# Kernel optimization log

Hardware: AMD Instinct MI355X
Metric: run time of the kernel (lower is better)

## Reference

```python
import jax, jax.numpy as jnp
import numpy as np

B, T, K, H = 2, 2048, 1024, 16


def setup_inputs() -> dict:
    key = jax.random.key(0)
    ks = jax.random.split(key, 9)
    sc = 0.02
    return {
        "x": jax.random.normal(ks[0], (B, T, K), dtype=jnp.float32),
        "Wq_w": jax.random.normal(ks[1], (K, K), dtype=jnp.float32) * sc,
        "Wq_b": jax.random.normal(ks[2], (K,), dtype=jnp.float32) * sc,
        "Wk_w": jax.random.normal(ks[3], (K, K), dtype=jnp.float32) * sc,
        "Wk_b": jax.random.normal(ks[4], (K,), dtype=jnp.float32) * sc,
        "Wv_w": jax.random.normal(ks[5], (K, K), dtype=jnp.float32) * sc,
        "Wv_b": jax.random.normal(ks[6], (K,), dtype=jnp.float32) * sc,
        "Wo_w": jax.random.normal(ks[7], (K, K), dtype=jnp.float32) * sc,
        "Wo_b": jax.random.normal(ks[8], (K,), dtype=jnp.float32) * sc,
    }


def reference(x, Wq_w, Wq_b, Wk_w, Wk_b, Wv_w, Wv_b, Wo_w, Wo_b):
    b, t, k = x.shape
    h = H
    s = k // h
    # nn.Linear: y = x @ W^T + b
    q = x @ Wq_w.T + Wq_b
    kk = x @ Wk_w.T + Wk_b
    v = x @ Wv_w.T + Wv_b
    # [b, t, h, s] -> [b, h, t, s]
    q = q.reshape(b, t, h, s).transpose(0, 2, 1, 3)
    kk = kk.reshape(b, t, h, s).transpose(0, 2, 1, 3)
    v = v.reshape(b, t, h, s).transpose(0, 2, 1, 3)
    # scores [b, h, t, t]
    dot = jnp.einsum("bhqd,bhkd->bhqk", q, kk)
    # causal mask: upper triangle (offset=1) set to -inf BEFORE scaling
    causal = jnp.tril(jnp.ones((t, t), dtype=bool))
    dot = jnp.where(causal, dot, -jnp.inf)
    # NOTE: original scales by sqrt(k) (full model dim), not sqrt(head_dim)
    dot = dot / jnp.sqrt(jnp.asarray(k, dot.dtype))
    attn = jax.nn.softmax(dot, axis=-1)
    out = jnp.einsum("bhqk,bhkd->bhqd", attn, v)  # [b, h, t, s]
    out = out.transpose(0, 2, 1, 3).reshape(b, t, k)
    return out @ Wo_w.T + Wo_b
```

## Files before the change

### kernel.cpp

```cpp
#include <hip/hip_runtime.h>

typedef unsigned short u16;
typedef unsigned int u32;
typedef __bf16 bf16x8 __attribute__((ext_vector_type(8)));
typedef float f32x4 __attribute__((ext_vector_type(4)));
typedef unsigned short u16x8 __attribute__((ext_vector_type(8)));

#define B_ 2
#define T_ 2048
#define K_ 1024
#define H_ 16
#define S_ 64
#define MKC 4194304
#define QSCALE 0.04508422f

__device__ __forceinline__ u16 f2bf(float f) {
  unsigned int u = __builtin_bit_cast(unsigned int, f);
  u += 0x7fffu + ((u >> 16) & 1u);
  return (u16)(u >> 16);
}

__device__ __forceinline__ f32x4 MFMA(bf16x8 a, bf16x8 b, f32x4 c) {
  return __builtin_amdgcn_mfma_f32_16x16x32_bf16(a, b, c, 0, 0, 0);
}

__device__ __forceinline__ void gld16(const void* g, void* l) {
  __builtin_amdgcn_global_load_lds((const __attribute__((address_space(1))) void*)g,
                                   (__attribute__((address_space(3))) void*)l, 16, 0, 0);
}

__global__ __launch_bounds__(256) void cvt_all(const float* __restrict__ x,
                                               const float* __restrict__ W0,
                                               const float* __restrict__ W1,
                                               const float* __restrict__ W2,
                                               const float* __restrict__ W3,
                                               u16* __restrict__ xb,
                                               u16* __restrict__ wb) {
  const int i = blockIdx.x * 256 + threadIdx.x;
  const float* src;
  u16* dst;
  if (i < 524288) {
    src = x + (size_t)i * 8;
    dst = xb + (size_t)i * 8;
  } else {
    const int j = i - 524288;
    const int sel = j >> 17;
    const float* W = sel == 0 ? W0 : sel == 1 ? W1 : sel == 2 ? W2 : W3;
    src = W + (size_t)(j & 131071) * 8;
    dst = wb + (size_t)j * 8;
  }
  const float4* s = (const float4*)src;
  float4 f0 = s[0], f1 = s[1];
  u16x8 p;
  p[0] = f2bf(f0.x); p[1] = f2bf(f0.y); p[2] = f2bf(f0.z); p[3] = f2bf(f0.w);
  p[4] = f2bf(f1.x); p[5] = f2bf(f1.y); p[6] = f2bf(f1.z); p[7] = f2bf(f1.w);
  *(u16x8*)dst = p;
}

template <int OMODE, int BN>
__global__ __launch_bounds__(256) void gemm16(const u16* __restrict__ A,
                                              const u16* __restrict__ Bm,
                                              const float* __restrict__ b0,
                                              const float* __restrict__ b1,
                                              const float* __restrict__ b2,
                                              void* __restrict__ C0,
                                              int M, int N, int K) {
  constexpr int NF = BN / 32;
  __shared__ u16 As[128 * 32];
  __shared__ u16 Bs[BN * 32];
  const int bm = blockIdx.x * 128;
  const int bn = blockIdx.y * BN;
  const int tid = threadIdx.x;
  const int w = tid >> 6, lane = tid & 63;
  const int wr = (w >> 1) * 64, wc = (w & 1) * (BN / 2);
  const int lr = lane & 15, g = lane >> 4;
  const int lk = g * 8;
  const int srow = lane >> 2, scol = (lane & 3) * 8;

  f32x4 acc[4][NF] = {};

  for (int k0 = 0; k0 < K; k0 += 32) {
#pragma unroll
    for (int i = 0; i < 2; ++i) {
      const int rbase = (i * 4 + w) * 16;
      gld16(A + (size_t)(bm + rbase + srow) * K + k0 + scol, &As[rbase * 32]);
    }
#pragma unroll
    for (int i = 0; i < BN / 64; ++i) {
      const int rbase = (i * 4 + w) * 16;
      gld16(Bm + (size_t)(bn + rbase + srow) * K + k0 + scol, &Bs[rbase * 32]);
    }
    asm volatile("s_waitcnt vmcnt(0)" ::: "memory");
    __syncthreads();
    bf16x8 af[4], bfr[NF];
#pragma unroll
    for (int m = 0; m < 4; ++m)
      af[m] = *(const bf16x8*)&As[(wr + m * 16 + lr) * 32 + lk];
#pragma unroll
    for (int n = 0; n < NF; ++n)
      bfr[n] = *(const bf16x8*)&Bs[(wc + n * 16 + lr) * 32 + lk];
    __builtin_amdgcn_s_setprio(1);
#pragma unroll
    for (int m = 0; m < 4; ++m)
#pragma unroll
      for (int n = 0; n < NF; ++n)
        acc[m][n] = MFMA(af[m], bfr[n], acc[m][n]);
    __builtin_amdgcn_s_setprio(0);
    __syncthreads();
  }

  const int sel = (OMODE == 2) ? 0 : (bn >> 10);
  const float* bp = (OMODE == 2) ? b0 : (sel == 0 ? b0 : sel == 1 ? b1 : b2);
#pragma unroll
  for (int n = 0; n < NF; ++n) {
    const int col = bn + wc + n * 16 + lr;
    const float bv = bp[(OMODE == 2) ? col : (col & 1023)];
#pragma unroll
    for (int m = 0; m < 4; ++m) {
#pragma unroll
      for (int r = 0; r < 4; ++r) {
        const int row = bm + wr + m * 16 + g * 4 + r;
        float v = acc[m][n][r] + bv;
        if (OMODE == 2) {
          ((float*)C0)[(size_t)row * N + col] = v;
        } else {
          u16* dst = (u16*)C0;
          const int cc = col & 1023;
          if (sel == 2) {
            const int bb = row >> 11, t = row & 2047, hh = cc >> 6, ss = cc & 63;
            dst[(size_t)2 * MKC + (((size_t)(bb * H_ + hh) * S_ + ss) << 11) + t] = f2bf(v);
          } else {
            if (sel == 0) v *= QSCALE;
            dst[(size_t)sel * MKC + (size_t)row * 1024 + cc] = f2bf(v);
          }
        }
      }
    }
  }
}

__global__ __launch_bounds__(256) void attn_fwd(const u16* __restrict__ Q,
                                                const u16* __restrict__ Kb,
                                                const u16* __restrict__ Vt,
                                                u16* __restrict__ O) {
  __shared__ u16 Ks[2][64 * 64];
  __shared__ u16 Vs[2][64 * 64];
  __shared__ u32 Ps[4][16 * 32];
  const int tid = threadIdx.x;
  const int w = tid >> 6, lane = tid & 63;
  const int qh = lane & 15;
  const int g = lane >> 4;
  const int bh = blockIdx.x;
  const int b = bh >> 4, h = bh & 15;
  const int yy = blockIdx.y, t7 = yy & 7, kq = yy >> 3;
  const int qtile = (kq == 0) ? t7 : (kq == 1) ? (15 - t7) : (kq == 2) ? (16 + t7) : (31 - t7);
  const int qb = qtile * 64;
  const int qw = qb + w * 16;
  const int myq = qw + qh;

  const size_t qoff = (size_t)(b * T_ + qw + qh) * K_ + h * S_ + g * 8;
  const bf16x8 bq0 = *(const bf16x8*)(Q + qoff);
  const bf16x8 bq1 = *(const bf16x8*)(Q + qoff + 32);

  const int srow = lane >> 3;
  const int sslot = (lane & 7) ^ srow;
  auto stage = [&](int buf, int k0) {
#pragma unroll
    for (int i = 0; i < 2; ++i) {
      const int rbase = w * 16 + i * 8;
      gld16(Kb + (size_t)(b * T_ + k0 + rbase + srow) * K_ + h * S_ + sslot * 8,
            &Ks[buf][rbase * 64]);
      gld16(Vt + (size_t)(bh * S_ + rbase + srow) * T_ + k0 + sslot * 8,
            &Vs[buf][rbase * 64]);
    }
  };

  const int nk = qtile + 1;
  stage(0, 0);
  asm volatile("s_waitcnt vmcnt(0)" ::: "memory");
  __syncthreads();

  float m = -INFINITY, lsum = 0.f;
  f32x4 o[4] = {};
  u32* pr = &Ps[w][qh * 32];
  const int sx = (qh & 7) << 2;
  const int ksw = qh & 7;

  for (int kt = 0; kt < nk; ++kt) {
    const int k0 = kt * 64;
    const int cur = kt & 1;
    if (kt + 1 < nk) stage(cur ^ 1, k0 + 64);

    f32x4 s[4] = {};
    __builtin_amdgcn_s_setprio(1);
#pragma unroll
    for (int a = 0; a < 4; ++a) {
      const u16* kr = &Ks[cur][(a * 16 + qh) * 64];
      const bf16x8 kf0 = *(const bf16x8*)(kr + ((g ^ ksw) * 8));
      const bf16x8 kf1 = *(const bf16x8*)(kr + (((4 + g) ^ ksw) * 8));
      s[a] = MFMA(kf0, bq0, s[a]);
      s[a] = MFMA(kf1, bq1, s[a]);
    }
    __builtin_amdgcn_s_setprio(0);

    float p[4][4];
    float vmax = -INFINITY;
    if (k0 + 63 > qw) {
#pragma unroll
      for (int a = 0; a < 4; ++a)
#pragma unroll
        for (int r = 0; r < 4; ++r) {
          const int kv = k0 + a * 16 + g * 4 + r;
          const float v = (kv <= myq) ? s[a][r] : -INFINITY;
          p[a][r] = v;
          vmax = fmaxf(vmax, v);
        }
    } else {
#pragma unroll
      for (int a = 0; a < 4; ++a)
#pragma unroll
        for (int r = 0; r < 4; ++r) {
          p[a][r] = s[a][r];
          vmax = fmaxf(vmax, s[a][r]);
        }
    }
    vmax = fmaxf(vmax, __shfl_xor(vmax, 16));
    vmax = fmaxf(vmax, __shfl_xor(vmax, 32));

    if (__any(vmax > m + 11.5f)) {
      const float mnew = fmaxf(m, vmax);
      const float alpha = __builtin_amdgcn_exp2f(m - mnew);
      m = mnew;
      lsum *= alpha;
      float aR[4];
#pragma unroll
      for (int r = 0; r < 4; ++r) aR[r] = __shfl(alpha, 4 * g + r);
#pragma unroll
      for (int n = 0; n < 4; ++n)
#pragma unroll
        for (int r = 0; r < 4; ++r) o[n][r] *= aR[r];
    }

    float ls = 0.f;
#pragma unroll
    for (int a = 0; a < 4; ++a)
#pragma unroll
      for (int r = 0; r < 4; ++r) {
        p[a][r] = __builtin_amdgcn_exp2f(p[a][r] - m);
        ls += p[a][r];
      }
    ls += __shfl_xor(ls, 16);
    ls += __shfl_xor(ls, 32);
    lsum += ls;

#pragma unroll
    for (int a = 0; a < 4; ++a) {
      u32 u0, u1;
      asm("v_cvt_pk_bf16_f32 %0, %1, %2" : "=v"(u0) : "v"(p[a][0]), "v"(p[a][1]));
      asm("v_cvt_pk_bf16_f32 %0, %1, %2" : "=v"(u1) : "v"(p[a][2]), "v"(p[a][3]));
      uint2 uu; uu.x = u0; uu.y = u1;
      *(uint2*)&pr[(8 * a + 2 * g) ^ sx] = uu;
    }
    __builtin_amdgcn_s_setprio(1);
#pragma unroll
    for (int c = 0; c < 2; ++c) {
      const bf16x8 pa = *(const bf16x8*)&pr[(16 * c + 4 * g) ^ sx];
#pragma unroll
      for (int n = 0; n < 4; ++n) {
        const bf16x8 vf =
            *(const bf16x8*)(&Vs[cur][(16 * n + qh) * 64] + (((c * 4 + g) ^ ksw) * 8));
        o[n] = MFMA(pa, vf, o[n]);
      }
    }
    __builtin_amdgcn_s_setprio(0);

    asm volatile("s_waitcnt vmcnt(0)" ::: "memory");
    __syncthreads();
  }

  const float inv = 1.f / lsum;
  float iR[4];
#pragma unroll
  for (int r = 0; r < 4; ++r) iR[r] = __shfl(inv, 4 * g + r);
#pragma unroll
  for (int r = 0; r < 4; ++r) {
    const size_t row = (size_t)(b * T_ + qw + 4 * g + r);
#pragma unroll
    for (int n = 0; n < 4; ++n)
      O[row * K_ + h * S_ + n * 16 + qh] = f2bf(o[n][r] * iR[r]);
  }
}

extern "C" void kernel_launch(void* const* d_in, const int* in_sizes, int n_in,
                              void* d_out, int out_size, void* d_ws, size_t ws_size,
                              hipStream_t stream) {
  (void)in_sizes; (void)n_in; (void)out_size; (void)ws_size;
  const float* x  = (const float*)d_in[0];
  const float* Wq = (const float*)d_in[1];
  const float* bq = (const float*)d_in[2];
  const float* Wk = (const float*)d_in[3];
  const float* bk = (const float*)d_in[4];
  const float* Wv = (const float*)d_in[5];
  const float* bv = (const float*)d_in[6];
  const float* Wo = (const float*)d_in[7];
  const float* bo = (const float*)d_in[8];
  float* out = (float*)d_out;

  const size_t MK = (size_t)MKC;
  const size_t WK = (size_t)K_ * K_;
  u16* Qb  = (u16*)d_ws;
  u16* Kbf = Qb + MK;
  u16* Vtb = Kbf + MK;
  u16* AO  = Vtb + MK;
  u16* xb  = AO + MK;
  u16* Wqkv = xb + MK;
  u16* Wob  = Wqkv + 3 * WK;

  dim3 blk(256);
  cvt_all<<<dim3(4096), blk, 0, stream>>>(x, Wq, Wk, Wv, Wo, xb, Wqkv);
  gemm16<3, 128><<<dim3(32, 24), blk, 0, stream>>>(xb, Wqkv, bq, bk, bv, Qb,
                                                   B_ * T_, 3 * K_, K_);
  attn_fwd<<<dim3(B_ * H_, T_ / 64), blk, 0, stream>>>(Qb, Kbf, Vtb, AO);
  gemm16<2, 64><<<dim3(32, 16), blk, 0, stream>>>(AO, Wob, bo, bo, bo, out,
                                                  B_ * T_, K_, K_);
}
```

Before: 116.3 us.

## Double-buffer GEMM shared tiles and widen attention KV tile to 128

After: 116.4 us. About the same (+0.0%).

```diff
diff --git a/kernel.cpp b/kernel.cpp
--- a/kernel.cpp
+++ b/kernel.cpp
@@ -66,8 +66,8 @@
                                               void* __restrict__ C0,
                                               int M, int N, int K) {
   constexpr int NF = BN / 32;
-  __shared__ u16 As[128 * 32];
-  __shared__ u16 Bs[BN * 32];
+  __shared__ u16 As[2][128 * 32];
+  __shared__ u16 Bs[2][BN * 32];
   const int bm = blockIdx.x * 128;
   const int bn = blockIdx.y * BN;
   const int tid = threadIdx.x;
@@ -79,33 +79,39 @@
 
   f32x4 acc[4][NF] = {};
 
-  for (int k0 = 0; k0 < K; k0 += 32) {
+  auto stg = [&](int buf, int k0) {
 #pragma unroll
     for (int i = 0; i < 2; ++i) {
       const int rbase = (i * 4 + w) * 16;
-      gld16(A + (size_t)(bm + rbase + srow) * K + k0 + scol, &As[rbase * 32]);
+      gld16(A + (size_t)(bm + rbase + srow) * K + k0 + scol, &As[buf][rbase * 32]);
     }
 #pragma unroll
     for (int i = 0; i < BN / 64; ++i) {
       const int rbase = (i * 4 + w) * 16;
-      gld16(Bm + (size_t)(bn + rbase + srow) * K + k0 + scol, &Bs[rbase * 32]);
-    }
-    asm volatile("s_waitcnt vmcnt(0)" ::: "memory");
-    __syncthreads();
+      gld16(Bm + (size_t)(bn + rbase + srow) * K + k0 + scol, &Bs[buf][rbase * 32]);
+    }
+  };
+
+  stg(0, 0);
+  asm volatile("s_waitcnt vmcnt(0)" ::: "memory");
+  __syncthreads();
+
+  for (int k0 = 0; k0 < K; k0 += 32) {
+    const int buf = (k0 >> 5) & 1;
+    if (k0 + 32 < K) stg(buf ^ 1, k0 + 32);
     bf16x8 af[4], bfr[NF];
 #pragma unroll
     for (int m = 0; m < 4; ++m)
-      af[m] = *(const bf16x8*)&As[(wr + m * 16 + lr) * 32 + lk];
+      af[m] = *(const bf16x8*)&As[buf][(wr + m * 16 + lr) * 32 + lk];
 #pragma unroll
     for (int n = 0; n < NF; ++n)
-      bfr[n] = *(const bf16x8*)&Bs[(wc + n * 16 + lr) * 32 + lk];
-    __builtin_amdgcn_s_setprio(1);
+      bfr[n] = *(const bf16x8*)&Bs[buf][(wc + n * 16 + lr) * 32 + lk];
 #pragma unroll
     for (int m = 0; m < 4; ++m)
 #pragma unroll
       for (int n = 0; n < NF; ++n)
         acc[m][n] = MFMA(af[m], bfr[n], acc[m][n]);
-    __builtin_amdgcn_s_setprio(0);
+    asm volatile("s_waitcnt vmcnt(0)" ::: "memory");
     __syncthreads();
   }
 
@@ -143,9 +149,9 @@
                                                 const u16* __restrict__ Kb,
                                                 const u16* __restrict__ Vt,
                                                 u16* __restrict__ O) {
-  __shared__ u16 Ks[2][64 * 64];
-  __shared__ u16 Vs[2][64 * 64];
-  __shared__ u32 Ps[4][16 * 32];
+  __shared__ u16 Ks[2][128 * 64];
+  __shared__ u16 Vs[2][64 * 128];
+  __shared__ u32 Ps[4][16 * 64];
   const int tid = threadIdx.x;
   const int w = tid >> 6, lane = tid & 63;
   const int qh = lane & 15;
@@ -153,7 +159,7 @@
   const int bh = blockIdx.x;
   const int b = bh >> 4, h = bh & 15;
   const int yy = blockIdx.y, t7 = yy & 7, kq = yy >> 3;
-  const int qtile = (kq == 0) ? t7 : (kq == 1) ? (15 - t7) : (kq == 2) ? (16 + t7) : (31 - t7);
+  const int qtile = (kq == 0) ? t7 : (kq == 1) ? (31 - t7) : (kq == 2) ? (8 + t7) : (23 - t7);
   const int qb = qtile * 64;
   const int qw = qb + w * 16;
   const int myq = qw + qh;
@@ -162,66 +168,73 @@
   const bf16x8 bq0 = *(const bf16x8*)(Q + qoff);
   const bf16x8 bq1 = *(const bf16x8*)(Q + qoff + 32);
 
-  const int srow = lane >> 3;
-  const int sslot = (lane & 7) ^ srow;
+  const int krow = lane >> 3;
+  const int kslot = (lane & 7) ^ krow;
+  const int vrow = lane >> 4;
   auto stage = [&](int buf, int k0) {
 #pragma unroll
-    for (int i = 0; i < 2; ++i) {
-      const int rbase = w * 16 + i * 8;
-      gld16(Kb + (size_t)(b * T_ + k0 + rbase + srow) * K_ + h * S_ + sslot * 8,
-            &Ks[buf][rbase * 64]);
-      gld16(Vt + (size_t)(bh * S_ + rbase + srow) * T_ + k0 + sslot * 8,
-            &Vs[buf][rbase * 64]);
+    for (int i = 0; i < 4; ++i) {
+      const int rb = w * 32 + i * 8;
+      gld16(Kb + (size_t)(b * T_ + k0 + rb + krow) * K_ + h * S_ + kslot * 8,
+            &Ks[buf][rb * 64]);
+    }
+#pragma unroll
+    for (int i = 0; i < 4; ++i) {
+      const int rb = w * 16 + i * 4;
+      const int row7 = ((i & 1) << 2) | vrow;
+      const int ss = (lane & 15) ^ row7;
+      gld16(Vt + (size_t)(bh * S_ + rb + vrow) * T_ + k0 + ss * 8,
+            &Vs[buf][rb * 128]);
     }
   };
 
-  const int nk = qtile + 1;
+  const int nk = (qb + 191) >> 7;
   stage(0, 0);
   asm volatile("s_waitcnt vmcnt(0)" ::: "memory");
   __syncthreads();
 
   float m = -INFINITY, lsum = 0.f;
   f32x4 o[4] = {};
-  u32* pr = &Ps[w][qh * 32];
+  u32* pr = &Ps[w][qh * 64];
   const int sx = (qh & 7) << 2;
   const int ksw = qh & 7;
 
   for (int kt = 0; kt < nk; ++kt) {
-    const int k0 = kt * 64;
+    const int k0 = kt * 128;
     const int cur = kt & 1;
-    if (kt + 1 < nk) stage(cur ^ 1, k0 + 64);
-
-    f32x4 s[4] = {};
+    if (kt + 1 < nk) stage(cur ^ 1, k0 + 128);
+
+    f32x4 s[8];
     __builtin_amdgcn_s_setprio(1);
 #pragma unroll
-    for (int a = 0; a < 4; ++a) {
+    for (int a = 0; a < 8; ++a) {
       const u16* kr = &Ks[cur][(a * 16 + qh) * 64];
       const bf16x8 kf0 = *(const bf16x8*)(kr + ((g ^ ksw) * 8));
       const bf16x8 kf1 = *(const bf16x8*)(kr + (((4 + g) ^ ksw) * 8));
-      s[a] = MFMA(kf0, bq0, s[a]);
-      s[a] = MFMA(kf1, bq1, s[a]);
+      f32x4 z = {0.f, 0.f, 0.f, 0.f};
+      z = MFMA(kf0, bq0, z);
+      s[a] = MFMA(kf1, bq1, z);
     }
     __builtin_amdgcn_s_setprio(0);
 
-    float p[4][4];
+    float p[8][4];
     float vmax = -INFINITY;
-    if (k0 + 63 > qw) {
-#pragma unroll
-      for (int a = 0; a < 4; ++a)
+    if (k0 + 127 > qw) {
+#pragma unroll
+      for (int a = 0; a < 8; ++a)
 #pragma unroll
         for (int r = 0; r < 4; ++r) {
           const int kv = k0 + a * 16 + g * 4 + r;
-          const float v = (kv <= myq) ? s[a][r] : -INFINITY;
-          p[a][r] = v;
-          vmax = fmaxf(vmax, v);
+          p[a][r] = (kv <= myq) ? s[a][r] : -INFINITY;
+          vmax = fmaxf(vmax, p[a][r]);
         }
     } else {
 #pragma unroll
-      for (int a = 0; a < 4; ++a)
+      for (int a = 0; a < 8; ++a)
 #pragma unroll
         for (int r = 0; r < 4; ++r) {
           p[a][r] = s[a][r];
-          vmax = fmaxf(vmax, s[a][r]);
+          vmax = fmaxf(vmax, p[a][r]);
         }
     }
     vmax = fmaxf(vmax, __shfl_xor(vmax, 16));
@@ -243,7 +256,7 @@
 
     float ls = 0.f;
 #pragma unroll
-    for (int a = 0; a < 4; ++a)
+    for (int a = 0; a < 8; ++a)
 #pragma unroll
       for (int r = 0; r < 4; ++r) {
         p[a][r] = __builtin_amdgcn_exp2f(p[a][r] - m);
@@ -254,7 +267,7 @@
     lsum += ls;
 
 #pragma unroll
-    for (int a = 0; a < 4; ++a) {
+    for (int a = 0; a < 8; ++a) {
       u32 u0, u1;
       asm("v_cvt_pk_bf16_f32 %0, %1, %2" : "=v"(u0) : "v"(p[a][0]), "v"(p[a][1]));
       asm("v_cvt_pk_bf16_f32 %0, %1, %2" : "=v"(u1) : "v"(p[a][2]), "v"(p[a][3]));
@@ -263,12 +276,12 @@
     }
     __builtin_amdgcn_s_setprio(1);
 #pragma unroll
-    for (int c = 0; c < 2; ++c) {
+    for (int c = 0; c < 4; ++c) {
       const bf16x8 pa = *(const bf16x8*)&pr[(16 * c + 4 * g) ^ sx];
 #pragma unroll
       for (int n = 0; n < 4; ++n) {
         const bf16x8 vf =
-            *(const bf16x8*)(&Vs[cur][(16 * n + qh) * 64] + (((c * 4 + g) ^ ksw) * 8));
+            *(const bf16x8*)(&Vs[cur][(16 * n + qh) * 128] + (((c * 4 + g) ^ ksw) * 8));
         o[n] = MFMA(pa, vf, o[n]);
       }
     }
```

## Double-buffer GEMM loads, keep P in registers via permuted K rows

Applied to the files above, without the earlier changes.

Result: faster. 110.9 us (-4.7%).

```diff
diff --git a/kernel.cpp b/kernel.cpp
--- a/kernel.cpp
+++ b/kernel.cpp
@@ -5,6 +5,7 @@
 typedef __bf16 bf16x8 __attribute__((ext_vector_type(8)));
 typedef float f32x4 __attribute__((ext_vector_type(4)));
 typedef unsigned short u16x8 __attribute__((ext_vector_type(8)));
+typedef unsigned int u32x4 __attribute__((ext_vector_type(4)));
 
 #define B_ 2
 #define T_ 2048
@@ -27,6 +28,15 @@
 __device__ __forceinline__ void gld16(const void* g, void* l) {
   __builtin_amdgcn_global_load_lds((const __attribute__((address_space(1))) void*)g,
                                    (__attribute__((address_space(3))) void*)l, 16, 0, 0);
+}
+
+template <int N>
+__device__ __forceinline__ void waitv() {
+  asm volatile("s_waitcnt vmcnt(%0)" ::"i"(N) : "memory");
+}
+__device__ __forceinline__ void memfence_barrier() {
+  asm volatile("" ::: "memory");
+  __builtin_amdgcn_s_barrier();
 }
 
 __global__ __launch_bounds__(256) void cvt_all(const float* __restrict__ x,
@@ -66,8 +76,9 @@
                                               void* __restrict__ C0,
                                               int M, int N, int K) {
   constexpr int NF = BN / 32;
-  __shared__ u16 As[128 * 32];
-  __shared__ u16 Bs[BN * 32];
+  constexpr int SOPS = 2 + BN / 64;
+  __shared__ u16 As[2][128 * 32];
+  __shared__ u16 Bs[2][BN * 32];
   const int bm = blockIdx.x * 128;
   const int bn = blockIdx.y * BN;
   const int tid = threadIdx.x;
@@ -79,34 +90,44 @@
 
   f32x4 acc[4][NF] = {};
 
-  for (int k0 = 0; k0 < K; k0 += 32) {
+  auto stg = [&](int buf, int k0) {
 #pragma unroll
     for (int i = 0; i < 2; ++i) {
       const int rbase = (i * 4 + w) * 16;
-      gld16(A + (size_t)(bm + rbase + srow) * K + k0 + scol, &As[rbase * 32]);
+      gld16(A + (size_t)(bm + rbase + srow) * K + k0 + scol, &As[buf][rbase * 32]);
     }
 #pragma unroll
     for (int i = 0; i < BN / 64; ++i) {
       const int rbase = (i * 4 + w) * 16;
-      gld16(Bm + (size_t)(bn + rbase + srow) * K + k0 + scol, &Bs[rbase * 32]);
-    }
-    asm volatile("s_waitcnt vmcnt(0)" ::: "memory");
-    __syncthreads();
+      gld16(Bm + (size_t)(bn + rbase + srow) * K + k0 + scol, &Bs[buf][rbase * 32]);
+    }
+  };
+
+  stg(0, 0);
+  const int NK = K >> 5;
+  for (int kk = 0; kk < NK; ++kk) {
+    const int buf = kk & 1;
+    const bool pf = (kk + 1 < NK);
+    if (pf) {
+      stg(buf ^ 1, (kk + 1) * 32);
+      waitv<SOPS>();
+    } else {
+      waitv<0>();
+    }
+    __builtin_amdgcn_s_barrier();
     bf16x8 af[4], bfr[NF];
 #pragma unroll
     for (int m = 0; m < 4; ++m)
-      af[m] = *(const bf16x8*)&As[(wr + m * 16 + lr) * 32 + lk];
+      af[m] = *(const bf16x8*)&As[buf][(wr + m * 16 + lr) * 32 + lk];
 #pragma unroll
     for (int n = 0; n < NF; ++n)
-      bfr[n] = *(const bf16x8*)&Bs[(wc + n * 16 + lr) * 32 + lk];
-    __builtin_amdgcn_s_setprio(1);
+      bfr[n] = *(const bf16x8*)&Bs[buf][(wc + n * 16 + lr) * 32 + lk];
 #pragma unroll
     for (int m = 0; m < 4; ++m)
 #pragma unroll
       for (int n = 0; n < NF; ++n)
         acc[m][n] = MFMA(af[m], bfr[n], acc[m][n]);
-    __builtin_amdgcn_s_setprio(0);
-    __syncthreads();
+    memfence_barrier();
   }
 
   const int sel = (OMODE == 2) ? 0 : (bn >> 10);
@@ -145,7 +166,6 @@
                                                 u16* __restrict__ O) {
   __shared__ u16 Ks[2][64 * 64];
   __shared__ u16 Vs[2][64 * 64];
-  __shared__ u32 Ps[4][16 * 32];
   const int tid = threadIdx.x;
   const int w = tid >> 6, lane = tid & 63;
   const int qh = lane & 15;
@@ -153,7 +173,8 @@
   const int bh = blockIdx.x;
   const int b = bh >> 4, h = bh & 15;
   const int yy = blockIdx.y, t7 = yy & 7, kq = yy >> 3;
-  const int qtile = (kq == 0) ? t7 : (kq == 1) ? (15 - t7) : (kq == 2) ? (16 + t7) : (31 - t7);
+  const int qtile = (kq == 0) ? (31 - t7) : (kq == 1) ? (16 + t7)
+                   : (kq == 2) ? (15 - t7) : t7;
   const int qb = qtile * 64;
   const int qw = qb + w * 16;
   const int myq = qw + qh;
@@ -163,43 +184,58 @@
   const bf16x8 bq1 = *(const bf16x8*)(Q + qoff + 32);
 
   const int srow = lane >> 3;
-  const int sslot = (lane & 7) ^ srow;
+  const int sl8 = ((lane & 7) ^ srow) * 8;
+  int kvp[2];
+#pragma unroll
+  for (int i = 0; i < 2; ++i) {
+    const int rho = w * 16 + i * 8 + srow;
+    const int a = rho >> 4;
+    kvp[i] = ((a >> 1) << 5) | (((rho >> 2) & 3) << 3) | ((a & 1) << 2) | (rho & 3);
+  }
   auto stage = [&](int buf, int k0) {
 #pragma unroll
     for (int i = 0; i < 2; ++i) {
-      const int rbase = w * 16 + i * 8;
-      gld16(Kb + (size_t)(b * T_ + k0 + rbase + srow) * K_ + h * S_ + sslot * 8,
-            &Ks[buf][rbase * 64]);
-      gld16(Vt + (size_t)(bh * S_ + rbase + srow) * T_ + k0 + sslot * 8,
-            &Vs[buf][rbase * 64]);
+      const int rb = w * 16 + i * 8;
+      gld16(Kb + (size_t)(b * T_ + k0 + kvp[i]) * K_ + h * S_ + sl8,
+            &Ks[buf][rb * 64]);
+    }
+#pragma unroll
+    for (int i = 0; i < 2; ++i) {
+      const int rb = w * 16 + i * 8;
+      gld16(Vt + (size_t)(bh * S_ + rb + srow) * T_ + k0 + sl8,
+            &Vs[buf][rb * 64]);
     }
   };
 
   const int nk = qtile + 1;
   stage(0, 0);
-  asm volatile("s_waitcnt vmcnt(0)" ::: "memory");
-  __syncthreads();
 
   float m = -INFINITY, lsum = 0.f;
   f32x4 o[4] = {};
-  u32* pr = &Ps[w][qh * 32];
-  const int sx = (qh & 7) << 2;
   const int ksw = qh & 7;
 
   for (int kt = 0; kt < nk; ++kt) {
     const int k0 = kt * 64;
     const int cur = kt & 1;
-    if (kt + 1 < nk) stage(cur ^ 1, k0 + 64);
-
-    f32x4 s[4] = {};
+    const bool pf = (kt + 1 < nk);
+    if (pf) {
+      stage(cur ^ 1, k0 + 64);
+      waitv<4>();
+    } else {
+      waitv<0>();
+    }
+    __builtin_amdgcn_s_barrier();
+
+    f32x4 s[4];
     __builtin_amdgcn_s_setprio(1);
 #pragma unroll
     for (int a = 0; a < 4; ++a) {
       const u16* kr = &Ks[cur][(a * 16 + qh) * 64];
       const bf16x8 kf0 = *(const bf16x8*)(kr + ((g ^ ksw) * 8));
       const bf16x8 kf1 = *(const bf16x8*)(kr + (((4 + g) ^ ksw) * 8));
-      s[a] = MFMA(kf0, bq0, s[a]);
-      s[a] = MFMA(kf1, bq1, s[a]);
+      f32x4 z = {0.f, 0.f, 0.f, 0.f};
+      z = MFMA(kf0, bq0, z);
+      s[a] = MFMA(kf1, bq1, z);
     }
     __builtin_amdgcn_s_setprio(0);
 
@@ -210,10 +246,9 @@
       for (int a = 0; a < 4; ++a)
 #pragma unroll
         for (int r = 0; r < 4; ++r) {
-          const int kv = k0 + a * 16 + g * 4 + r;
-          const float v = (kv <= myq) ? s[a][r] : -INFINITY;
-          p[a][r] = v;
-          vmax = fmaxf(vmax, v);
+          const int kv = k0 + ((a >> 1) << 5) + (g << 3) + ((a & 1) << 2) + r;
+          p[a][r] = (kv <= myq) ? s[a][r] : -INFINITY;
+          vmax = fmaxf(vmax, p[a][r]);
         }
     } else {
 #pragma unroll
@@ -221,7 +256,7 @@
 #pragma unroll
         for (int r = 0; r < 4; ++r) {
           p[a][r] = s[a][r];
-          vmax = fmaxf(vmax, s[a][r]);
+          vmax = fmaxf(vmax, p[a][r]);
         }
     }
     vmax = fmaxf(vmax, __shfl_xor(vmax, 16));
@@ -253,18 +288,16 @@
     ls += __shfl_xor(ls, 32);
     lsum += ls;
 
-#pragma unroll
-    for (int a = 0; a < 4; ++a) {
-      u32 u0, u1;
-      asm("v_cvt_pk_bf16_f32 %0, %1, %2" : "=v"(u0) : "v"(p[a][0]), "v"(p[a][1]));
-      asm("v_cvt_pk_bf16_f32 %0, %1, %2" : "=v"(u1) : "v"(p[a][2]), "v"(p[a][3]));
-      uint2 uu; uu.x = u0; uu.y = u1;
-      *(uint2*)&pr[(8 * a + 2 * g) ^ sx] = uu;
-    }
     __builtin_amdgcn_s_setprio(1);
 #pragma unroll
     for (int c = 0; c < 2; ++c) {
-      const bf16x8 pa = *(const bf16x8*)&pr[(16 * c + 4 * g) ^ sx];
+      u32 t0, t1, t2, t3;
+      asm("v_cvt_pk_bf16_f32 %0, %1, %2" : "=v"(t0) : "v"(p[2 * c][0]), "v"(p[2 * c][1]));
+      asm("v_cvt_pk_bf16_f32 %0, %1, %2" : "=v"(t1) : "v"(p[2 * c][2]), "v"(p[2 * c][3]));
+      asm("v_cvt_pk_bf16_f32 %0, %1, %2" : "=v"(t2) : "v"(p[2 * c + 1][0]), "v"(p[2 * c + 1][1]));
+      asm("v_cvt_pk_bf16_f32 %0, %1, %2" : "=v"(t3) : "v"(p[2 * c + 1][2]), "v"(p[2 * c + 1][3]));
+      u32x4 tv; tv[0] = t0; tv[1] = t1; tv[2] = t2; tv[3] = t3;
+      const bf16x8 pa = __builtin_bit_cast(bf16x8, tv);
 #pragma unroll
       for (int n = 0; n < 4; ++n) {
         const bf16x8 vf =
@@ -274,8 +307,7 @@
     }
     __builtin_amdgcn_s_setprio(0);
 
-    asm volatile("s_waitcnt vmcnt(0)" ::: "memory");
-    __syncthreads();
+    memfence_barrier();
   }
 
   const float inv = 1.f / lsum;
```
